# Optimization experiments

Hardware: AMD Instinct MI355X
Metric: run time of the kernel (lower is better)

The kernel has to match this reference:

```python
import jax, jax.numpy as jnp
import numpy as np

HORIZON = 1024
N_EMBD = 256
N_LAYER = 4
ACTION_DIM = 10
DIM = 64
ACT_NUM = 10
N_POS = 4 * (1 + HORIZON)
FEAT = 3 + DIM * ACT_NUM + ACTION_DIM  # 653
EPS = 1e-5
BATCH = 8


def _layernorm(x, g, b):
    m = jnp.mean(x, axis=-1, keepdims=True)
    v = jnp.mean((x - m) ** 2, axis=-1, keepdims=True)
    return (x - m) * jax.lax.rsqrt(v + EPS) * g + b


def setup_inputs() -> dict:
    key = jax.random.key(0)
    ks = jax.random.split(key, 16)
    f = jnp.float32
    L, E = N_LAYER, N_EMBD
    return {
        'query_states': jax.random.normal(ks[0], (BATCH, 64), f),
        'action_set': jax.random.normal(ks[1], (BATCH, ACT_NUM, DIM), f),
        'context_actions': jax.random.normal(ks[2], (BATCH, HORIZON, ACTION_DIM), f),
        'context_rewards': jax.random.normal(ks[3], (BATCH, HORIZON, 1), f),
        'W_embed': jax.random.normal(ks[4], (FEAT, E), f) * 0.02,
        'b_embed': jnp.zeros((E,), f),
        'wpe': jax.random.normal(ks[5], (N_POS, E), f) * 0.02,
        'Wq': jax.random.normal(ks[6], (L, E, E), f) * 0.02,
        'Wk': jax.random.normal(ks[7], (L, E, E), f) * 0.02,
        'Wv': jax.random.normal(ks[8], (L, E, E), f) * 0.02,
        'ln1_g': jnp.ones((L, E), f),
        'ln1_b': jnp.zeros((L, E), f),
        'W1': jax.random.normal(ks[9], (L, E, E), f) * 0.02,
        'b1': jnp.zeros((L, E), f),
        'W2': jax.random.normal(ks[10], (L, E, E), f) * 0.02,
        'b2': jnp.zeros((L, E), f),
        'ln2_g': jnp.ones((L, E), f),
        'ln2_b': jnp.zeros((L, E), f),
        'W_pred': jax.random.normal(ks[11], (E, ACTION_DIM), f) * 0.02,
        'b_pred': jnp.zeros((ACTION_DIM,), f),
    }


def reference(query_states, action_set, context_actions, context_rewards,
              W_embed, b_embed, wpe, Wq, Wk, Wv,
              ln1_g, ln1_b, W1, b1, W2, b2, ln2_g, ln2_b,
              W_pred, b_pred):
    B = action_set.shape[0]
    T = context_actions.shape[1]
    A = context_actions.shape[2]
    N = 2 * T
    # --- build the interleaved sequence (test=False path) ---
    aset0 = action_set.reshape(B, 1, -1)                         # [B,1,dim*act_num]
    aset = jnp.concatenate([aset0, jnp.zeros_like(aset0)], axis=1)  # [B,2,F0]
    aset = jnp.tile(aset, (1, T, 1))                              # [B,2T,F0]
    action_seq = jnp.zeros((B, N, A + 1), dtype=context_actions.dtype)
    action_seq = action_seq.at[:, 1::2, :].set(
        jnp.concatenate([context_actions, context_rewards], axis=2))
    one_seq = jnp.ones((B, N, 1), dtype=context_actions.dtype)
    pos_seq = jnp.broadcast_to(
        jnp.arange(1, N + 1, dtype=context_actions.dtype).reshape(1, N, 1), (B, N, 1))
    seq = jnp.concatenate([aset, action_seq, one_seq, pos_seq], axis=2)  # [B,N,FEAT]
    # --- embed + positional embedding ---
    H = seq @ W_embed + b_embed          # [B,N,E]
    H = H + wpe[:N]                       # position_ids = arange(N)
    # --- causal mask with per-row 1/(i+1) normalization ---
    i = jnp.arange(N)[:, None]
    j = jnp.arange(N)[None, :]
    mask = jnp.where(j <= i, 1.0 / (i + 1).astype(H.dtype), 0.0)  # [N,N]
    # --- decoder layers: relu(QK^T)*mask attention + MLP, layernorms ---
    for l in range(N_LAYER):
        q = H @ Wq[l]
        k = H @ Wk[l]
        v = H @ Wv[l]
        attn = jax.nn.relu(jnp.einsum('bid,bjd->bij', q, k)) * mask  # [B,N,N]
        H = H + jnp.einsum('bij,bjd->bid', attn, v)
        H = _layernorm(H, ln1_g[l], ln1_b[l])
        H = H + jax.nn.relu(H @ W1[l] + b1[l]) @ W2[l] + b2[l]
        H = _layernorm(H, ln2_g[l], ln2_b[l])
    preds = H @ W_pred + b_pred           # [B,N,action_dim]
    return preds[:, 0::2, :]              # [B,T,action_dim]
```

## Files before the change

kernel.cpp:

```cpp
#include <hip/hip_runtime.h>


#define BB 8
#define TT 1024
#define NN 2048
#define EE 256
#define LL 4

typedef __attribute__((ext_vector_type(8))) short short8;
typedef __attribute__((ext_vector_type(4))) float f32x4;

__device__ inline ushort f2b(float f) {
    union { float f; unsigned u; } x; x.f = f;
    unsigned u = x.u;
    return (ushort)((u + 0x7fffu + ((u >> 16) & 1u)) >> 16);
}
__device__ inline unsigned cvtpk(float lo, float hi) {
    unsigned r;
    asm volatile("v_cvt_pk_bf16_f32 %0, %1, %2" : "=v"(r) : "v"(lo), "v"(hi));
    return r;
}
__device__ inline size_t pk256(int row, int k) {
    return ((size_t)((row >> 4) * 8 + (k >> 5))) * 512
         + (size_t)((((k >> 3) & 3) * 16 + (row & 15)) * 8 + (k & 7));
}
__device__ inline size_t vpk_idx(int bb, int nn, int e) {
    return ((size_t)(bb*64 + (nn >> 5)) * 16 + (e >> 4)) * 512
         + (size_t)((((nn >> 3) & 3) * 16 + (e & 15)) * 8 + (nn & 7));
}

__global__ __launch_bounds__(256) void wprep_k(
    const float* __restrict__ Wq, const float* __restrict__ Wk,
    const float* __restrict__ Wv, const float* __restrict__ W1,
    const float* __restrict__ W2,
    ushort* __restrict__ WQKt, ushort* __restrict__ WVt,
    ushort* __restrict__ W1t, ushort* __restrict__ W2t)
{
    int id = blockIdx.x;
    int m = id >> 4, t = id & 15;
    int l = m / 5, which = m % 5;
    const float* src; ushort* dst;
    size_t o = (size_t)l * 65536;
    switch (which) {
        case 0: src = Wq + o; dst = WQKt + (size_t)l*131072;          break;
        case 1: src = Wk + o; dst = WQKt + (size_t)l*131072 + 65536;  break;
        case 2: src = Wv + o; dst = WVt + o; break;
        case 3: src = W1 + o; dst = W1t + o; break;
        default: src = W2 + o; dst = W2t + o; break;
    }
    int tk = (t >> 2) * 64;
    int tn = (t & 3) * 64;
    __shared__ ushort T[64][68];
    int tid = threadIdx.x;
    int r = tid >> 4, c4 = (tid & 15) * 4;
    #pragma unroll
    for (int it = 0; it < 4; ++it) {
        int k = r + it*16;
        float4 v = *(const float4*)&src[(size_t)(tk + k)*256 + tn + c4];
        T[k][c4+0] = f2b(v.x); T[k][c4+1] = f2b(v.y);
        T[k][c4+2] = f2b(v.z); T[k][c4+3] = f2b(v.w);
    }
    __syncthreads();
    #pragma unroll
    for (int it = 0; it < 4; ++it) {
        int n = tn + r + it*16;
        int k0 = tk + c4;
        ushort4 ov;
        ov.x = T[c4+0][n-tn]; ov.y = T[c4+1][n-tn];
        ov.z = T[c4+2][n-tn]; ov.w = T[c4+3][n-tn];
        *(ushort4*)&dst[pk256(n, k0)] = ov;
    }
}

__global__ __launch_bounds__(256) void base_even_k(
    const float* __restrict__ aset, const float* __restrict__ We,
    const float* __restrict__ be, float* __restrict__ BE)
{
    int b = blockIdx.x; int e = threadIdx.x;
    __shared__ float as[640];
    for (int i = e; i < 640; i += 256) as[i] = aset[b*640 + i];
    __syncthreads();
    float s = We[651*EE + e] + be[e];
    for (int f = 0; f < 640; ++f) s = fmaf(as[f], We[f*EE + e], s);
    BE[b*EE + e] = s;
}

__global__ __launch_bounds__(256) void embed_k(
    const float* __restrict__ BE, const float* __restrict__ ca,
    const float* __restrict__ cr, const float* __restrict__ We,
    const float* __restrict__ be, const float* __restrict__ wpe,
    float* __restrict__ H, ushort* __restrict__ Hbf)
{
    int e = threadIdx.x;
    #pragma unroll
    for (int k = 0; k < 8; ++k) {
        int rb = blockIdx.x * 8 + k;
        int b = rb >> 11, n = rb & (NN-1);
        float h;
        if ((n & 1) == 0) {
            h = BE[b*EE + e];
        } else {
            int t = n >> 1;
            h = We[651*EE + e] + be[e];
            const float* cap = ca + (size_t)(b*TT + t)*10;
            #pragma unroll
            for (int i = 0; i < 10; ++i) h = fmaf(cap[i], We[(640+i)*EE + e], h);
            h = fmaf(cr[b*TT + t], We[650*EE + e], h);
        }
        h = fmaf((float)(n + 1), We[652*EE + e], h);
        h += wpe[(size_t)n*EE + e];
        H[(size_t)rb*EE + e] = h;
        Hbf[pk256(rb, e)] = f2b(h);
    }
}

__global__ __launch_bounds__(256, 2) void qkv_k(
    const ushort* __restrict__ A, const ushort* __restrict__ WQK,
    const ushort* __restrict__ WV,
    ushort* __restrict__ Qo, ushort* __restrict__ Ko, ushort* __restrict__ Vo)
{
    int tid = threadIdx.x;
    int w = tid >> 6, l = tid & 63;
    int lr = l & 15, lg = l >> 4;
    int wr = w >> 1, wc = w & 1;
    int rt0 = blockIdx.x * 8 + wr*4;
    int ct0 = blockIdx.y * 8 + wc*4;
    const ushort* Ap = A + (size_t)rt0*4096 + l*8;
    const ushort* Bp = (blockIdx.y < 4 ? WQK + (size_t)ct0*4096
                                       : WV + (size_t)(ct0-32)*4096) + l*8;
    f32x4 acc[4][4];
    #pragma unroll
    for (int i = 0; i < 4; ++i)
        #pragma unroll
        for (int j = 0; j < 4; ++j) acc[i][j] = (f32x4){0.f,0.f,0.f,0.f};
    #pragma unroll
    for (int kc = 0; kc < 8; ++kc) {
        short8 af[4], bf[4];
        #pragma unroll
        for (int rg = 0; rg < 4; ++rg) af[rg] = *(const short8*)(Ap + (size_t)rg*4096 + kc*512);
        #pragma unroll
        for (int cg = 0; cg < 4; ++cg) bf[cg] = *(const short8*)(Bp + (size_t)cg*4096 + kc*512);
        #pragma unroll
        for (int rg = 0; rg < 4; ++rg)
            #pragma unroll
            for (int cg = 0; cg < 4; ++cg)
                acc[rg][cg] = __builtin_amdgcn_mfma_f32_16x16x32_bf16(af[rg], bf[cg], acc[rg][cg], 0,0,0);
    }
    #pragma unroll
    for (int rg = 0; rg < 4; ++rg)
        #pragma unroll
        for (int cg = 0; cg < 4; ++cg)
            #pragma unroll
            for (int r = 0; r < 4; ++r) {
                int row = rt0*16 + rg*16 + lg*4 + r;
                int col = ct0*16 + cg*16 + lr;
                ushort xv = f2b(acc[rg][cg][r]);
                if (col < 256)      Qo[pk256(row, col)] = xv;
                else if (col < 512) Ko[pk256(row, col - 256)] = xv;
                else {
                    int e = col - 512, bb = row >> 11, nn = row & (NN-1);
                    Vo[vpk_idx(bb, nn, e)] = xv;
                }
            }
}

__global__ __launch_bounds__(512, 2) void attn_k(
    const ushort* Qp, const ushort* __restrict__ Kp,
    const ushort* __restrict__ Vp, const float* H,
    const float* __restrict__ g, const float* __restrict__ bt,
    const ushort* __restrict__ W1t, const float* __restrict__ b1p,
    const ushort* __restrict__ W2t, const float* __restrict__ b2p,
    const float* __restrict__ g2, const float* __restrict__ bt2,
    float* Hout, ushort* __restrict__ Hpk)
{
    int blk = blockIdx.x;
    int pk = blk >> 3, b = blk & 7;
    int tid = threadIdx.x;
    int w = tid >> 6, l = tid & 63;
    int lr = l & 15, lg = l >> 4;
    int sel  = (w & 1) ^ ((w >> 2) & 1);
    int part = w >> 1;
    int s  = sel ? (127 - pk) : pk;
    int i0 = s * 16;
    int NT = (s >> 1) + 1;
    int j0 = (part * NT) >> 2;
    int j1 = ((part + 1) * NT) >> 2;

    __shared__ float comb[2][5440];
    __shared__ ushort ylds[2][4096];
    __shared__ float red2[2][16][4][2];

    const ushort* Qt    = Qp + ((size_t)(b*128 + s)) * 4096 + l*8;
    const ushort* Kbase = Kp + (size_t)(b*128) * 4096 + l*8;
    const ushort* Vbase = Vp + (size_t)(b*64) * 16 * 512 + l*8;

    short8 qb[8];
    #pragma unroll
    for (int kc = 0; kc < 8; ++kc) qb[kc] = *(const short8*)(Qt + kc*512);

    f32x4 oacc[16];
    #pragma unroll
    for (int et = 0; et < 16; ++et) oacc[et] = (f32x4){0.f,0.f,0.f,0.f};

    int ig = i0 + lr;
    for (int jt = j0; jt < j1; ++jt) {
        const ushort* Kt = Kbase + (size_t)(jt*2) * 4096;
        short8 ka0[8], ka1[8];
        #pragma unroll
        for (int kc = 0; kc < 8; ++kc) {
            ka0[kc] = *(const short8*)(Kt + kc*512);
            ka1[kc] = *(const short8*)(Kt + 4096 + kc*512);
        }
        const ushort* Vt = Vbase + (size_t)(jt*16) * 512;
        short8 vf[16];
        #pragma unroll
        for (int et = 0; et < 16; ++et)
            vf[et] = *(const short8*)(Vt + et*512);
        f32x4 c0a = {0.f,0.f,0.f,0.f}, c0b = {0.f,0.f,0.f,0.f};
        f32x4 c1a = {0.f,0.f,0.f,0.f}, c1b = {0.f,0.f,0.f,0.f};
        #pragma unroll
        for (int kc = 0; kc < 8; kc += 2) {
            c0a = __builtin_amdgcn_mfma_f32_16x16x32_bf16(ka0[kc],   qb[kc],   c0a, 0,0,0);
            c0b = __builtin_amdgcn_mfma_f32_16x16x32_bf16(ka0[kc+1], qb[kc+1], c0b, 0,0,0);
            c1a = __builtin_amdgcn_mfma_f32_16x16x32_bf16(ka1[kc],   qb[kc],   c1a, 0,0,0);
            c1b = __builtin_amdgcn_mfma_f32_16x16x32_bf16(ka1[kc+1], qb[kc+1], c1b, 0,0,0);
        }
        f32x4 c0 = c0a + c0b, c1 = c1a + c1b;
        #pragma unroll
        for (int r = 0; r < 4; ++r) {
            int jg = jt*32 + lg*4 + r;
            c0[r] = (jg <= ig) ? fmaxf(c0[r], 0.f) : 0.f;
            c1[r] = (jg + 16 <= ig) ? fmaxf(c1[r], 0.f) : 0.f;
        }
        unsigned u0 = cvtpk(c0[0], c0[1]), u1 = cvtpk(c0[2], c0[3]);
        unsigned u2 = cvtpk(c1[0], c1[1]), u3 = cvtpk(c1[2], c1[3]);
        int srcA = 32*(lg & 1) + lr;
        int srcB = srcA + 16;
        unsigned a0A = __shfl((int)u0, srcA), a1A = __shfl((int)u1, srcA);
        unsigned a0B = __shfl((int)u0, srcB), a1B = __shfl((int)u1, srcB);
        unsigned b0A = __shfl((int)u2, srcA), b1A = __shfl((int)u3, srcA);
        unsigned b0B = __shfl((int)u2, srcB), b1B = __shfl((int)u3, srcB);
        bool lo = (lg < 2);
        union { unsigned u[4]; short8 v; } sv;
        sv.u[0] = lo ? a0A : b0A;
        sv.u[1] = lo ? a1A : b1A;
        sv.u[2] = lo ? a0B : b0B;
        sv.u[3] = lo ? a1B : b1B;
        short8 sa = sv.v;
        __builtin_amdgcn_s_setprio(1);
        #pragma unroll
        for (int et = 0; et < 16; ++et)
            oacc[et] = __builtin_amdgcn_mfma_f32_16x16x32_bf16(sa, vf[et], oacc[et], 0,0,0);
        __builtin_amdgcn_s_setprio(0);
    }

    float* cb = &comb[sel][0];
    #pragma unroll
    for (int rnd = 1; rnd <= 3; ++rnd) {
        if (part == rnd) {
            #pragma unroll
            for (int et = 0; et < 16; ++et)
                #pragma unroll
                for (int r = 0; r < 4; ++r) {
                    int idx = et*340 + l*5 + r;
                    float v = oacc[et][r];
                    if (rnd == 1) cb[idx] = v; else cb[idx] += v;
                }
        }
        __syncthreads();
    }
    if (part == 0) {
        float sm[4] = {0.f,0.f,0.f,0.f}, sq[4] = {0.f,0.f,0.f,0.f};
        #pragma unroll
        for (int et = 0; et < 16; ++et)
            #pragma unroll
            for (int r = 0; r < 4; ++r) {
                int irow = i0 + lg*4 + r;
                size_t base = ((size_t)(b*NN + irow))*EE + et*16 + lr;
                float x = H[base] + (oacc[et][r] + cb[et*340 + l*5 + r])
                                    * (1.0f / (float)(irow + 1));
                oacc[et][r] = x;
                sm[r] += x; sq[r] += x*x;
            }
        #pragma unroll
        for (int off = 1; off < 16; off <<= 1)
            #pragma unroll
            for (int r = 0; r < 4; ++r) {
                sm[r] += __shfl_xor(sm[r], off);
                sq[r] += __shfl_xor(sq[r], off);
            }
        float mean[4], inv[4];
        #pragma unroll
        for (int r = 0; r < 4; ++r) {
            mean[r] = sm[r] * (1.0f/256.0f);
            float var = sq[r] * (1.0f/256.0f) - mean[r]*mean[r];
            inv[r] = 1.0f / sqrtf(var + 1e-5f);
        }
        ushort* yl = &ylds[sel][0];
        #pragma unroll
        for (int et = 0; et < 16; ++et) {
            int col = et*16 + lr;
            float gv = g[col], bv = bt[col];
            #pragma unroll
            for (int r = 0; r < 4; ++r) {
                int row16 = lg*4 + r;
                float y = (oacc[et][r] - mean[r]) * inv[r] * gv + bv;
                cb[row16*256 + col] = y;
                int idx = (col >> 5)*512 + ((((col >> 3) & 3) << 4) + row16)*8
                        + (col & 7);
                yl[idx] = f2b(y);
            }
        }
    }
    __syncthreads();
    f32x4 macc[4];
    {
        const ushort* Ay = &ylds[sel][0] + l*8;
        const ushort* Bp = W1t + (size_t)(part*4)*4096 + l*8;
        #pragma unroll
        for (int cg = 0; cg < 4; ++cg) macc[cg] = (f32x4){0.f,0.f,0.f,0.f};
        #pragma unroll
        for (int kc = 0; kc < 8; ++kc) {
            short8 af = *(const short8*)(Ay + kc*512);
            #pragma unroll
            for (int cg = 0; cg < 4; ++cg) {
                short8 bf = *(const short8*)(Bp + (size_t)cg*4096 + kc*512);
                macc[cg] = __builtin_amdgcn_mfma_f32_16x16x32_bf16(af, bf, macc[cg], 0,0,0);
            }
        }
    }
    __syncthreads();
    {
        ushort* yl = &ylds[sel][0];
        #pragma unroll
        for (int cg = 0; cg < 4; ++cg)
            #pragma unroll
            for (int r = 0; r < 4; ++r) {
                int col = part*64 + cg*16 + lr;
                int row16 = lg*4 + r;
                float x = fmaxf(macc[cg][r] + b1p[col], 0.f);
                int idx = (col >> 5)*512 + ((((col >> 3) & 3) << 4) + row16)*8
                        + (col & 7);
                yl[idx] = f2b(x);
            }
    }
    __syncthreads();
    float x2[4][4];
    {
        const ushort* Am = &ylds[sel][0] + l*8;
        const ushort* Bp = W2t + (size_t)(part*4)*4096 + l*8;
        f32x4 m2[4];
        #pragma unroll
        for (int cg = 0; cg < 4; ++cg) m2[cg] = (f32x4){0.f,0.f,0.f,0.f};
        #pragma unroll
        for (int kc = 0; kc < 8; ++kc) {
            short8 af = *(const short8*)(Am + kc*512);
            #pragma unroll
            for (int cg = 0; cg < 4; ++cg) {
                short8 bf = *(const short8*)(Bp + (size_t)cg*4096 + kc*512);
                m2[cg] = __builtin_amdgcn_mfma_f32_16x16x32_bf16(af, bf, m2[cg], 0,0,0);
            }
        }
        float sm2[4] = {0.f,0.f,0.f,0.f}, sq2[4] = {0.f,0.f,0.f,0.f};
        #pragma unroll
        for (int cg = 0; cg < 4; ++cg)
            #pragma unroll
            for (int r = 0; r < 4; ++r) {
                int col = part*64 + cg*16 + lr;
                int row16 = lg*4 + r;
                float v = m2[cg][r] + b2p[col] + cb[row16*256 + col];
                x2[cg][r] = v;
                sm2[r] += v; sq2[r] += v*v;
            }
        #pragma unroll
        for (int off = 1; off < 16; off <<= 1)
            #pragma unroll
            for (int r = 0; r < 4; ++r) {
                sm2[r] += __shfl_xor(sm2[r], off);
                sq2[r] += __shfl_xor(sq2[r], off);
            }
        if (lr == 0) {
            #pragma unroll
            for (int r = 0; r < 4; ++r) {
                red2[sel][lg*4 + r][part][0] = sm2[r];
                red2[sel][lg*4 + r][part][1] = sq2[r];
            }
        }
    }
    __syncthreads();
    {
        float mean[4], inv[4];
        #pragma unroll
        for (int r = 0; r < 4; ++r) {
            int row16 = lg*4 + r;
            float S  = red2[sel][row16][0][0] + red2[sel][row16][1][0]
                     + red2[sel][row16][2][0] + red2[sel][row16][3][0];
            float S2 = red2[sel][row16][0][1] + red2[sel][row16][1][1]
                     + red2[sel][row16][2][1] + red2[sel][row16][3][1];
            mean[r] = S * (1.0f/256.0f);
            float var = S2 * (1.0f/256.0f) - mean[r]*mean[r];
            inv[r] = 1.0f / sqrtf(var + 1e-5f);
        }
        #pragma unroll
        for (int cg = 0; cg < 4; ++cg) {
            int col = part*64 + cg*16 + lr;
            float gv = g2[col], bv = bt2[col];
            #pragma unroll
            for (int r = 0; r < 4; ++r) {
                int irow = i0 + lg*4 + r;
                size_t base = ((size_t)(b*NN + irow))*EE + col;
                float y2 = (x2[cg][r] - mean[r]) * inv[r] * gv + bv;
                Hout[base] = y2;
                Hpk[pk256(b*NN + irow, col)] = f2b(y2);
            }
        }
    }
}

__global__ __launch_bounds__(256) void pred_k(
    const float* __restrict__ H, const float* __restrict__ Wp,
    const float* __restrict__ bp, float* __restrict__ out)
{
    int bt = blockIdx.x;
    int b = bt >> 10, t = bt & 1023;
    size_t row = (size_t)b*NN + 2*t;
    __shared__ float hs[256];
    __shared__ float pr[16][16];
    int tid = threadIdx.x;
    hs[tid] = H[row*EE + tid];
    __syncthreads();
    int c = tid & 15, seg = tid >> 4;
    float p = 0.f;
    if (c < 10) {
        #pragma unroll
        for (int e2 = 0; e2 < 16; ++e2)
            p = fmaf(hs[seg*16 + e2], Wp[(seg*16 + e2)*10 + c], p);
    }
    pr[seg][c] = p;
    __syncthreads();
    if (tid < 10) {
        float sacc = bp[tid];
        #pragma unroll
        for (int k2 = 0; k2 < 16; ++k2) sacc += pr[k2][tid];
        out[(size_t)bt*10 + tid] = sacc;
    }
}

extern "C" void kernel_launch(void* const* d_in, const int* in_sizes, int n_in,
                              void* d_out, int out_size, void* d_ws, size_t ws_size,
                              hipStream_t stream)
{
    const float* action_set = (const float*)d_in[1];
    const float* ctx_act    = (const float*)d_in[2];
    const float* ctx_rew    = (const float*)d_in[3];
    const float* W_embed    = (const float*)d_in[4];
    const float* b_embed    = (const float*)d_in[5];
    const float* wpe        = (const float*)d_in[6];
    const float* Wq         = (const float*)d_in[7];
    const float* Wk         = (const float*)d_in[8];
    const float* Wv         = (const float*)d_in[9];
    const float* ln1g       = (const float*)d_in[10];
    const float* ln1b       = (const float*)d_in[11];
    const float* W1         = (const float*)d_in[12];
    const float* b1         = (const float*)d_in[13];
    const float* W2         = (const float*)d_in[14];
    const float* b2         = (const float*)d_in[15];
    const float* ln2g       = (const float*)d_in[16];
    const float* ln2b       = (const float*)d_in[17];
    const float* Wp         = (const float*)d_in[18];
    const float* bp         = (const float*)d_in[19];
    float* out = (float*)d_out;

    float* ws = (float*)d_ws;
    const size_t SZ = (size_t)BB*NN*EE;
    size_t o = 0;
    float*  Hb   = ws;               o += SZ;
    ushort* Hbf  = (ushort*)(ws+o);  o += SZ/2;
    ushort* Qp   = (ushort*)(ws+o);  o += SZ/2;
    ushort* Kpk  = (ushort*)(ws+o);  o += SZ/2;
    ushort* Vpk  = (ushort*)(ws+o);  o += SZ/2;
    ushort* WQKt = (ushort*)(ws+o);  o += 262144;
    ushort* WVt  = (ushort*)(ws+o);  o += 131072;
    ushort* W1t  = (ushort*)(ws+o);  o += 131072;
    ushort* W2t  = (ushort*)(ws+o);  o += 131072;
    float*  BE   = ws + o;

    wprep_k<<<320, 256, 0, stream>>>(Wq, Wk, Wv, W1, W2, WQKt, WVt, W1t, W2t);
    base_even_k<<<BB, 256, 0, stream>>>(action_set, W_embed, b_embed, BE);
    embed_k<<<BB*NN/8, 256, 0, stream>>>(BE, ctx_act, ctx_rew, W_embed, b_embed, wpe, Hb, Hbf);

    for (int l = 0; l < LL; ++l) {
        qkv_k<<<dim3(128, 6), 256, 0, stream>>>(
            Hbf, WQKt + (size_t)l*131072, WVt + (size_t)l*65536, Qp, Kpk, Vpk);
        attn_k<<<512, 512, 0, stream>>>(
            Qp, Kpk, Vpk, Hb, ln1g + l*EE, ln1b + l*EE,
            W1t + (size_t)l*65536, b1 + l*EE,
            W2t + (size_t)l*65536, b2 + l*EE,
            ln2g + l*EE, ln2b + l*EE, Hb, Hbf);
    }
    pred_k<<<BB*TT, 256, 0, stream>>>(Hb, Wp, bp, out);
}
```

Baseline: 399.6 us.

## Compute only even rows in final layer attention and MLP

Adds a specialized last-layer attention+MLP kernel that processes only the even sequence rows, since only those feed the prediction output. Each block handles 32 rows spread by stride 2 (16 active rows) with 8 waves splitting the key range, so attention, layernorm and MLP work for odd rows is skipped in layer 4. It also pads the shared-memory row stride to 258 to reduce bank conflicts, and makes the prediction kernel process 4 rows per block. The Q fragment load now gathers strided rows, and the split across 8 waves adds more reduction rounds through shared memory.

Result: faster. 379.3 us (-5.1%).

```diff
diff --git a/kernel.cpp b/kernel.cpp
--- a/kernel.cpp
+++ b/kernel.cpp
@@ -6,6 +6,7 @@
 #define NN 2048
 #define EE 256
 #define LL 4
+#define YST 258
 
 typedef __attribute__((ext_vector_type(8))) short short8;
 typedef __attribute__((ext_vector_type(4))) float f32x4;
@@ -190,13 +191,15 @@
     __shared__ ushort ylds[2][4096];
     __shared__ float red2[2][16][4][2];
 
-    const ushort* Qt    = Qp + ((size_t)(b*128 + s)) * 4096 + l*8;
     const ushort* Kbase = Kp + (size_t)(b*128) * 4096 + l*8;
     const ushort* Vbase = Vp + (size_t)(b*64) * 16 * 512 + l*8;
 
     short8 qb[8];
-    #pragma unroll
-    for (int kc = 0; kc < 8; ++kc) qb[kc] = *(const short8*)(Qt + kc*512);
+    {
+        const ushort* Qt = Qp + ((size_t)(b*128 + s)) * 4096 + l*8;
+        #pragma unroll
+        for (int kc = 0; kc < 8; ++kc) qb[kc] = *(const short8*)(Qt + kc*512);
+    }
 
     f32x4 oacc[16];
     #pragma unroll
@@ -305,7 +308,7 @@
             for (int r = 0; r < 4; ++r) {
                 int row16 = lg*4 + r;
                 float y = (oacc[et][r] - mean[r]) * inv[r] * gv + bv;
-                cb[row16*256 + col] = y;
+                cb[row16*YST + col] = y;
                 int idx = (col >> 5)*512 + ((((col >> 3) & 3) << 4) + row16)*8
                         + (col & 7);
                 yl[idx] = f2b(y);
@@ -368,7 +371,7 @@
             for (int r = 0; r < 4; ++r) {
                 int col = part*64 + cg*16 + lr;
                 int row16 = lg*4 + r;
-                float v = m2[cg][r] + b2p[col] + cb[row16*256 + col];
+                float v = m2[cg][r] + b2p[col] + cb[row16*YST + col];
                 x2[cg][r] = v;
                 sm2[r] += v; sq2[r] += v*v;
             }
@@ -417,32 +420,292 @@
     }
 }
 
+__global__ __launch_bounds__(512, 2) void attn_even_k(
+    const ushort* Qp, const ushort* __restrict__ Kp,
+    const ushort* __restrict__ Vp, const float* H,
+    const float* __restrict__ g, const float* __restrict__ bt,
+    const ushort* __restrict__ W1t, const float* __restrict__ b1p,
+    const ushort* __restrict__ W2t, const float* __restrict__ b2p,
+    const float* __restrict__ g2, const float* __restrict__ bt2,
+    float* Hout, ushort* __restrict__ Hpk)
+{
+    int bk = blockIdx.x;
+    int half = bk >> 8;
+    int idx8 = bk & 255;
+    int pk = idx8 >> 3, b = idx8 & 7;
+    int sv = half ? (63 - pk) : pk;
+    int tid = threadIdx.x;
+    int part = tid >> 6, l = tid & 63;
+    int lr = l & 15, lg = l >> 4;
+    int i0 = sv * 32;
+    int NT = sv + 1;
+    int j0 = (part * NT) >> 3;
+    int j1 = ((part + 1) * NT) >> 3;
+
+    __shared__ float comb[5440];
+    __shared__ ushort ylds[4096];
+    __shared__ float red2[16][8][2];
+
+    const ushort* Kbase = Kp + (size_t)(b*128) * 4096 + l*8;
+    const ushort* Vbase = Vp + (size_t)(b*64) * 16 * 512 + l*8;
+
+    short8 qb[8];
+    {
+        const ushort* Qb0 = Qp + (size_t)(b*128) * 4096;
+        int qrow = i0 + 2*lr;
+        #pragma unroll
+        for (int kc = 0; kc < 8; ++kc)
+            qb[kc] = *(const short8*)&Qb0[pk256(qrow, kc*32 + lg*8)];
+    }
+
+    f32x4 oacc[16];
+    #pragma unroll
+    for (int et = 0; et < 16; ++et) oacc[et] = (f32x4){0.f,0.f,0.f,0.f};
+
+    int ig = i0 + 2*lr;
+    for (int jt = j0; jt < j1; ++jt) {
+        const ushort* Kt = Kbase + (size_t)(jt*2) * 4096;
+        short8 ka0[8], ka1[8];
+        #pragma unroll
+        for (int kc = 0; kc < 8; ++kc) {
+            ka0[kc] = *(const short8*)(Kt + kc*512);
+            ka1[kc] = *(const short8*)(Kt + 4096 + kc*512);
+        }
+        const ushort* Vt = Vbase + (size_t)(jt*16) * 512;
+        short8 vf[16];
+        #pragma unroll
+        for (int et = 0; et < 16; ++et)
+            vf[et] = *(const short8*)(Vt + et*512);
+        f32x4 c0a = {0.f,0.f,0.f,0.f}, c0b = {0.f,0.f,0.f,0.f};
+        f32x4 c1a = {0.f,0.f,0.f,0.f}, c1b = {0.f,0.f,0.f,0.f};
+        #pragma unroll
+        for (int kc = 0; kc < 8; kc += 2) {
+            c0a = __builtin_amdgcn_mfma_f32_16x16x32_bf16(ka0[kc],   qb[kc],   c0a, 0,0,0);
+            c0b = __builtin_amdgcn_mfma_f32_16x16x32_bf16(ka0[kc+1], qb[kc+1], c0b, 0,0,0);
+            c1a = __builtin_amdgcn_mfma_f32_16x16x32_bf16(ka1[kc],   qb[kc],   c1a, 0,0,0);
+            c1b = __builtin_amdgcn_mfma_f32_16x16x32_bf16(ka1[kc+1], qb[kc+1], c1b, 0,0,0);
+        }
+        f32x4 c0 = c0a + c0b, c1 = c1a + c1b;
+        #pragma unroll
+        for (int r = 0; r < 4; ++r) {
+            int jg = jt*32 + lg*4 + r;
+            c0[r] = (jg <= ig) ? fmaxf(c0[r], 0.f) : 0.f;
+            c1[r] = (jg + 16 <= ig) ? fmaxf(c1[r], 0.f) : 0.f;
+        }
+        unsigned u0 = cvtpk(c0[0], c0[1]), u1 = cvtpk(c0[2], c0[3]);
+        unsigned u2 = cvtpk(c1[0], c1[1]), u3 = cvtpk(c1[2], c1[3]);
+        int srcA = 32*(lg & 1) + lr;
+        int srcB = srcA + 16;
+        unsigned a0A = __shfl((int)u0, srcA), a1A = __shfl((int)u1, srcA);
+        unsigned a0B = __shfl((int)u0, srcB), a1B = __shfl((int)u1, srcB);
+        unsigned b0A = __shfl((int)u2, srcA), b1A = __shfl((int)u3, srcA);
+        unsigned b0B = __shfl((int)u2, srcB), b1B = __shfl((int)u3, srcB);
+        bool lo = (lg < 2);
+        union { unsigned u[4]; short8 v; } sv2;
+        sv2.u[0] = lo ? a0A : b0A;
+        sv2.u[1] = lo ? a1A : b1A;
+        sv2.u[2] = lo ? a0B : b0B;
+        sv2.u[3] = lo ? a1B : b1B;
+        short8 sa = sv2.v;
+        __builtin_amdgcn_s_setprio(1);
+        #pragma unroll
+        for (int et = 0; et < 16; ++et)
+            oacc[et] = __builtin_amdgcn_mfma_f32_16x16x32_bf16(sa, vf[et], oacc[et], 0,0,0);
+        __builtin_amdgcn_s_setprio(0);
+    }
+
+    #pragma unroll
+    for (int rnd = 1; rnd <= 7; ++rnd) {
+        if (part == rnd) {
+            #pragma unroll
+            for (int et = 0; et < 16; ++et)
+                #pragma unroll
+                for (int r = 0; r < 4; ++r) {
+                    int idx = et*340 + l*5 + r;
+                    float v = oacc[et][r];
+                    if (rnd == 1) comb[idx] = v; else comb[idx] += v;
+                }
+        }
+        __syncthreads();
+    }
+    if (part == 0) {
+        float sm[4] = {0.f,0.f,0.f,0.f}, sq[4] = {0.f,0.f,0.f,0.f};
+        #pragma unroll
+        for (int et = 0; et < 16; ++et)
+            #pragma unroll
+            for (int r = 0; r < 4; ++r) {
+                int irow = i0 + 2*(lg*4 + r);
+                size_t base = ((size_t)(b*NN + irow))*EE + et*16 + lr;
+                float x = H[base] + (oacc[et][r] + comb[et*340 + l*5 + r])
+                                    * (1.0f / (float)(irow + 1));
+                oacc[et][r] = x;
+                sm[r] += x; sq[r] += x*x;
+            }
+        #pragma unroll
+        for (int off = 1; off < 16; off <<= 1)
+            #pragma unroll
+            for (int r = 0; r < 4; ++r) {
+                sm[r] += __shfl_xor(sm[r], off);
+                sq[r] += __shfl_xor(sq[r], off);
+            }
+        float mean[4], inv[4];
+        #pragma unroll
+        for (int r = 0; r < 4; ++r) {
+            mean[r] = sm[r] * (1.0f/256.0f);
+            float var = sq[r] * (1.0f/256.0f) - mean[r]*mean[r];
+            inv[r] = 1.0f / sqrtf(var + 1e-5f);
+        }
+        #pragma unroll
+        for (int et = 0; et < 16; ++et) {
+            int col = et*16 + lr;
+            float gv = g[col], bv = bt[col];
+            #pragma unroll
+            for (int r = 0; r < 4; ++r) {
+                int row16 = lg*4 + r;
+                float y = (oacc[et][r] - mean[r]) * inv[r] * gv + bv;
+                comb[row16*YST + col] = y;
+                int idx = (col >> 5)*512 + ((((col >> 3) & 3) << 4) + row16)*8
+                        + (col & 7);
+                ylds[idx] = f2b(y);
+            }
+        }
+    }
+    __syncthreads();
+    f32x4 macc[2];
+    {
+        const ushort* Ay = &ylds[0] + l*8;
+        const ushort* Bp = W1t + (size_t)(part*2)*4096 + l*8;
+        #pragma unroll
+        for (int cg = 0; cg < 2; ++cg) macc[cg] = (f32x4){0.f,0.f,0.f,0.f};
+        #pragma unroll
+        for (int kc = 0; kc < 8; ++kc) {
+            short8 af = *(const short8*)(Ay + kc*512);
+            #pragma unroll
+            for (int cg = 0; cg < 2; ++cg) {
+                short8 bf = *(const short8*)(Bp + (size_t)cg*4096 + kc*512);
+                macc[cg] = __builtin_amdgcn_mfma_f32_16x16x32_bf16(af, bf, macc[cg], 0,0,0);
+            }
+        }
+    }
+    __syncthreads();
+    {
+        #pragma unroll
+        for (int cg = 0; cg < 2; ++cg)
+            #pragma unroll
+            for (int r = 0; r < 4; ++r) {
+                int col = part*32 + cg*16 + lr;
+                int row16 = lg*4 + r;
+                float x = fmaxf(macc[cg][r] + b1p[col], 0.f);
+                int idx = (col >> 5)*512 + ((((col >> 3) & 3) << 4) + row16)*8
+                        + (col & 7);
+                ylds[idx] = f2b(x);
+            }
+    }
+    __syncthreads();
+    float x2[2][4];
+    {
+        const ushort* Am = &ylds[0] + l*8;
+        const ushort* Bp = W2t + (size_t)(part*2)*4096 + l*8;
+        f32x4 m2[2];
+        #pragma unroll
+        for (int cg = 0; cg < 2; ++cg) m2[cg] = (f32x4){0.f,0.f,0.f,0.f};
+        #pragma unroll
+        for (int kc = 0; kc < 8; ++kc) {
+            short8 af = *(const short8*)(Am + kc*512);
+            #pragma unroll
+            for (int cg = 0; cg < 2; ++cg) {
+                short8 bf = *(const short8*)(Bp + (size_t)cg*4096 + kc*512);
+                m2[cg] = __builtin_amdgcn_mfma_f32_16x16x32_bf16(af, bf, m2[cg], 0,0,0);
+            }
+        }
+        float sm2[4] = {0.f,0.f,0.f,0.f}, sq2[4] = {0.f,0.f,0.f,0.f};
+        #pragma unroll
+        for (int cg = 0; cg < 2; ++cg)
+            #pragma unroll
+            for (int r = 0; r < 4; ++r) {
+                int col = part*32 + cg*16 + lr;
+                int row16 = lg*4 + r;
+                float v = m2[cg][r] + b2p[col] + comb[row16*YST + col];
+                x2[cg][r] = v;
+                sm2[r] += v; sq2[r] += v*v;
+            }
+        #pragma unroll
+        for (int off = 1; off < 16; off <<= 1)
+            #pragma unroll
+            for (int r = 0; r < 4; ++r) {
+                sm2[r] += __shfl_xor(sm2[r], off);
+                sq2[r] += __shfl_xor(sq2[r], off);
+            }
+        if (lr == 0) {
+            #pragma unroll
+            for (int r = 0; r < 4; ++r) {
+                red2[lg*4 + r][part][0] = sm2[r];
+                red2[lg*4 + r][part][1] = sq2[r];
+            }
+        }
+    }
+    __syncthreads();
+    {
+        float mean[4], inv[4];
+        #pragma unroll
+        for (int r = 0; r < 4; ++r) {
+            int row16 = lg*4 + r;
+            float S = 0.f, S2 = 0.f;
+            #pragma unroll
+            for (int p2 = 0; p2 < 8; ++p2) {
+                S  += red2[row16][p2][0];
+                S2 += red2[row16][p2][1];
+            }
+            mean[r] = S * (1.0f/256.0f);
+            float var = S2 * (1.0f/256.0f) - mean[r]*mean[r];
+            inv[r] = 1.0f / sqrtf(var + 1e-5f);
+        }
+        #pragma unroll
+        for (int cg = 0; cg < 2; ++cg) {
+            int col = part*32 + cg*16 + lr;
+            float gv = g2[col], bv = bt2[col];
+            #pragma unroll
+            for (int r = 0; r < 4; ++r) {
+                int irow = i0 + 2*(lg*4 + r);
+                size_t base = ((size_t)(b*NN + irow))*EE + col;
+                float y2 = (x2[cg][r] - mean[r]) * inv[r] * gv + bv;
+                Hout[base] = y2;
+                Hpk[pk256(b*NN + irow, col)] = f2b(y2);
+            }
+        }
+    }
+}
+
 __global__ __launch_bounds__(256) void pred_k(
     const float* __restrict__ H, const float* __restrict__ Wp,
     const float* __restrict__ bp, float* __restrict__ out)
 {
-    int bt = blockIdx.x;
-    int b = bt >> 10, t = bt & 1023;
-    size_t row = (size_t)b*NN + 2*t;
     __shared__ float hs[256];
     __shared__ float pr[16][16];
     int tid = threadIdx.x;
-    hs[tid] = H[row*EE + tid];
-    __syncthreads();
     int c = tid & 15, seg = tid >> 4;
-    float p = 0.f;
-    if (c < 10) {
-        #pragma unroll
-        for (int e2 = 0; e2 < 16; ++e2)
-            p = fmaf(hs[seg*16 + e2], Wp[(seg*16 + e2)*10 + c], p);
-    }
-    pr[seg][c] = p;
-    __syncthreads();
-    if (tid < 10) {
-        float sacc = bp[tid];
-        #pragma unroll
-        for (int k2 = 0; k2 < 16; ++k2) sacc += pr[k2][tid];
-        out[(size_t)bt*10 + tid] = sacc;
+    #pragma unroll
+    for (int ii = 0; ii < 4; ++ii) {
+        int bt = blockIdx.x * 4 + ii;
+        int b = bt >> 10, t = bt & 1023;
+        size_t row = (size_t)b*NN + 2*t;
+        hs[tid] = H[row*EE + tid];
+        __syncthreads();
+        float p = 0.f;
+        if (c < 10) {
+            #pragma unroll
+            for (int e2 = 0; e2 < 16; ++e2)
+                p = fmaf(hs[seg*16 + e2], Wp[(seg*16 + e2)*10 + c], p);
+        }
+        pr[seg][c] = p;
+        __syncthreads();
+        if (tid < 10) {
+            float sacc = bp[tid];
+            #pragma unroll
+            for (int k2 = 0; k2 < 16; ++k2) sacc += pr[k2][tid];
+            out[(size_t)bt*10 + tid] = sacc;
+        }
+        __syncthreads();
     }
 }
 
@@ -492,11 +755,19 @@
     for (int l = 0; l < LL; ++l) {
         qkv_k<<<dim3(128, 6), 256, 0, stream>>>(
             Hbf, WQKt + (size_t)l*131072, WVt + (size_t)l*65536, Qp, Kpk, Vpk);
-        attn_k<<<512, 512, 0, stream>>>(
-            Qp, Kpk, Vpk, Hb, ln1g + l*EE, ln1b + l*EE,
-            W1t + (size_t)l*65536, b1 + l*EE,
-            W2t + (size_t)l*65536, b2 + l*EE,
-            ln2g + l*EE, ln2b + l*EE, Hb, Hbf);
-    }
-    pred_k<<<BB*TT, 256, 0, stream>>>(Hb, Wp, bp, out);
-}
+        if (l < LL-1) {
+            attn_k<<<512, 512, 0, stream>>>(
+                Qp, Kpk, Vpk, Hb, ln1g + l*EE, ln1b + l*EE,
+                W1t + (size_t)l*65536, b1 + l*EE,
+                W2t + (size_t)l*65536, b2 + l*EE,
+                ln2g + l*EE, ln2b + l*EE, Hb, Hbf);
+        } else {
+            attn_even_k<<<512, 512, 0, stream>>>(
+                Qp, Kpk, Vpk, Hb, ln1g + l*EE, ln1b + l*EE,
+                W1t + (size_t)l*65536, b1 + l*EE,
+                W2t + (size_t)l*65536, b2 + l*EE,
+                ln2g + l*EE, ln2b + l*EE, Hb, Hbf);
+        }
+    }
+    pred_k<<<BB*TT/4, 256, 0, stream>>>(Hb, Wp, bp, out);
+}
```
